# Optimization experiments

Hardware: AMD Instinct MI355X
Metric: run time of the kernel (lower is better)

Reference implementation:

```python
import jax, jax.numpy as jnp
import numpy as np

B, N, IN_DIM, HID = 8, 2048, 128, 64
LN_EPS = 1e-5
NEG_INF = -9e15
LRELU_SLOPE = 0.2


def setup_inputs() -> dict:
    key = jax.random.key(0)
    k1, k2, k3, k4, k5, k6 = jax.random.split(key, 6)
    stdv = 1.0 / np.sqrt(HID)
    adj = jax.random.randint(k1, (B, N, N), 0, 2, dtype=jnp.int32)
    # ensure self-loops so every row has at least one valid entry
    adj = adj.at[:, jnp.arange(N), jnp.arange(N)].set(1)
    return {
        "adj": adj,
        "x": jax.random.normal(k2, (B, N, IN_DIM), dtype=jnp.float32),
        "h": jax.random.normal(k3, (B, N, HID), dtype=jnp.float32),
        "X2H": jax.random.uniform(k4, (IN_DIM, 3 * HID), minval=-stdv, maxval=stdv, dtype=jnp.float32),
        "H2H": jax.random.uniform(k5, (HID, 3 * HID), minval=-stdv, maxval=stdv, dtype=jnp.float32),
        "a": jax.random.uniform(k6, (2 * HID, 1), minval=-stdv, maxval=stdv, dtype=jnp.float32),
    }


def _gated_inputs(x, h, X2H, H2H):
    gate_x = x @ X2H          # [B,N,3H]
    gate_h = h @ H2H          # [B,N,3H]
    i_r, i_i, i_n = jnp.split(gate_x, 3, axis=2)
    h_r, h_i, h_n = jnp.split(gate_h, 3, axis=2)
    resetgate = jax.nn.sigmoid(i_r + h_r)
    inputgate = jax.nn.sigmoid(i_i + h_i)
    irh = i_n + resetgate * h_n
    mu = jnp.mean(irh, axis=-1, keepdims=True)
    var = jnp.mean(jnp.square(irh - mu), axis=-1, keepdims=True)
    irh = (irh - mu) * jax.lax.rsqrt(var + LN_EPS)  # layer_norm, no affine
    newgate = jnp.tanh(irh)
    return newgate + inputgate * (h - newgate)


def reference(adj, x, h, X2H, H2H, a):
    Wh = _gated_inputs(x, h, X2H, H2H)              # [B,N,H]
    Wh1 = Wh @ a[:HID]                              # [B,N,1]
    Wh2 = Wh @ a[HID:]                              # [B,N,1]
    e = jax.nn.leaky_relu(Wh1 + jnp.swapaxes(Wh2, 1, 2), LRELU_SLOPE)  # [B,N,N]
    scores = jnp.where(adj != 0, e, jnp.float32(NEG_INF))
    attention = jax.nn.softmax(scores, axis=2)
    h_prime = attention @ Wh                        # [B,N,H]
    return (h_prime, Wh)
```

## Files before the change

kernel.cpp:

```cpp
#include <hip/hip_runtime.h>

constexpr int BB  = 8;
constexpr int NN  = 2048;
constexpr int IND = 128;
constexpr int HD  = 64;
constexpr float LN_EPS = 1e-5f;
constexpr float SLOPE  = 0.2f;

typedef _Float16 half8 __attribute__((ext_vector_type(8)));
typedef _Float16 half4 __attribute__((ext_vector_type(4)));
typedef float    f32x4 __attribute__((ext_vector_type(4)));

__device__ __forceinline__ float wave_sum(float v) {
    #pragma unroll
    for (int off = 32; off > 0; off >>= 1) v += __shfl_xor(v, off);
    return v;
}
__device__ __forceinline__ float wave_max(float v) {
    #pragma unroll
    for (int off = 32; off > 0; off >>= 1) v = fmaxf(v, __shfl_xor(v, off));
    return v;
}

__global__ void k_prep(const float* __restrict__ X2H, const float* __restrict__ H2H,
                       _Float16* __restrict__ Wt)
{
    const int tot = 256 * 192;
    for (int idx = blockIdx.x * 256 + threadIdx.x; idx < tot; idx += gridDim.x * 256) {
        const int col = idx / 192, k = idx % 192;
        float v;
        if (col < 128)       v = (k < 128) ? X2H[(size_t)k * 192 + col]
                                           : H2H[(size_t)(k - 128) * 192 + col];
        else if (col < 192)  v = (k < 128) ? X2H[(size_t)k * 192 + col] : 0.f;
        else                 v = (k >= 128) ? H2H[(size_t)(k - 128) * 192 + (col - 64)] : 0.f;
        Wt[idx] = (_Float16)v;
    }
}

__global__ __launch_bounds__(256, 4) void k_gates(
    const float* __restrict__ x, const float* __restrict__ h,
    const _Float16* __restrict__ Wt, const float* __restrict__ a,
    float* __restrict__ Wh_out, _Float16* __restrict__ Whh2,
    float* __restrict__ Wh1, float* __restrict__ Wh2)
{
    __shared__ float gbuf[16][260];

    const int tid = threadIdx.x, lane = tid & 63, w = tid >> 6;
    const int m = lane & 15, q = lane >> 4;
    const int row0 = blockIdx.x * 16;

    f32x4 acc[4];
    #pragma unroll
    for (int ct = 0; ct < 4; ++ct) acc[ct] = (f32x4){0.f, 0.f, 0.f, 0.f};

    #pragma unroll
    for (int kc = 0; kc < 6; ++kc) {
        half8 a8;
        if (kc < 4) {
            const float* xp = x + (size_t)(row0 + m) * IND + kc * 32 + q * 8;
            const f32x4 v0 = *(const f32x4*)xp;
            const f32x4 v1 = *(const f32x4*)(xp + 4);
            #pragma unroll
            for (int j = 0; j < 4; ++j) { a8[j] = (_Float16)v0[j]; a8[4 + j] = (_Float16)v1[j]; }
        } else {
            const float* hp_ = h + (size_t)(row0 + m) * HD + (kc - 4) * 32 + q * 8;
            const f32x4 v0 = *(const f32x4*)hp_;
            const f32x4 v1 = *(const f32x4*)(hp_ + 4);
            #pragma unroll
            for (int j = 0; j < 4; ++j) { a8[j] = (_Float16)v0[j]; a8[4 + j] = (_Float16)v1[j]; }
        }
        #pragma unroll
        for (int ct = 0; ct < 4; ++ct) {
            const half8 b8 = *(const half8*)(Wt + ((size_t)(w * 64 + ct * 16 + m) * 192 + kc * 32 + q * 8));
            acc[ct] = __builtin_amdgcn_mfma_f32_16x16x32_f16(a8, b8, acc[ct], 0, 0, 0);
        }
    }

    #pragma unroll
    for (int ct = 0; ct < 4; ++ct)
        #pragma unroll
        for (int r2 = 0; r2 < 4; ++r2)
            gbuf[q * 4 + r2][w * 64 + ct * 16 + m] = acc[ct][r2];
    __syncthreads();

    const float a0 = a[lane], a1 = a[64 + lane];
    half4 p4;
    const int grow0 = row0 + w * 4;
    #pragma unroll
    for (int r = 0; r < 4; ++r) {
        const int row = w * 4 + r;
        const int grow = row0 + row;
        const float g0 = gbuf[row][lane];
        const float g1 = gbuf[row][64 + lane];
        const float g2 = gbuf[row][128 + lane];
        const float g3 = gbuf[row][192 + lane];
        const float rg = 1.f / (1.f + __expf(-g0));
        const float ig = 1.f / (1.f + __expf(-g1));
        const float irh = g2 + rg * g3;
        const float mu = wave_sum(irh) * (1.f / 64.f);
        const float dv = irh - mu;
        const float var = wave_sum(dv * dv) * (1.f / 64.f);
        const float ng = tanhf(dv * rsqrtf(var + LN_EPS));
        const float hr = h[(size_t)grow * HD + lane];
        const float wh = ng + ig * (hr - ng);
        Wh_out[(size_t)grow * HD + lane] = wh;
        p4[r] = (_Float16)wh;
        const float d1 = wave_sum(wh * a0);
        const float d2 = wave_sum(wh * a1);
        if (lane == 0) { Wh1[grow] = d1; Wh2[grow] = d2; }
    }
    *(half4*)(Whh2 + ((size_t)(grow0 >> 3) * 64 + lane) * 8 + (w & 1) * 4) = p4;
}

__global__ __launch_bounds__(256) void k_aux(
    const float* __restrict__ Wh1, const float* __restrict__ Wh2,
    float* __restrict__ u, float* __restrict__ up,
    _Float16* __restrict__ v16, _Float16* __restrict__ v16p)
{
    __shared__ float red[4];
    const int tid = threadIdx.x, lane = tid & 63, w = tid >> 6;
    const int b = blockIdx.x >> 3, part = blockIdx.x & 7;

    float mx = -3e38f;
    #pragma unroll
    for (int k = 0; k < 8; ++k) mx = fmaxf(mx, Wh2[b * NN + k * 256 + tid]);
    mx = wave_max(mx);
    if (lane == 0) red[w] = mx;
    __syncthreads();
    const float M = fmaxf(fmaxf(red[0], red[1]), fmaxf(red[2], red[3]));

    const int grow = b * NN + part * 256 + tid;
    const float t0 = Wh1[grow] + M;
    const float c  = (t0 > 0.f) ? t0 : SLOPE * t0;
    u[grow]  = __expf(t0 - c);
    up[grow] = __expf(SLOPE * t0 - c);
    const float w2 = Wh2[grow] - M;
    v16[grow]  = (_Float16)__expf(w2);
    v16p[grow] = (_Float16)__expf(SLOPE * w2);
}

__global__ __launch_bounds__(256, 8) void k_score(
    const int* __restrict__ adj,
    const float* __restrict__ Wh1, const float* __restrict__ Wh2,
    unsigned short* __restrict__ Mb)
{
    const int tid = threadIdx.x;
    const int4* __restrict__ adj4 = (const int4*)adj;

    #pragma unroll
    for (int s = 0; s < 4; ++s) {
        const int row = s * 4096 + blockIdx.x;
        const int b   = row >> 11;
        const float negw1 = -Wh1[row];

        const int4 a0 = adj4[(size_t)row * 512 + tid * 2];
        const int4 a1 = adj4[(size_t)row * 512 + tid * 2 + 1];
        const f32x4 w0 = ((const f32x4*)(Wh2 + (size_t)b * NN))[tid * 2];
        const f32x4 w1 = ((const f32x4*)(Wh2 + (size_t)b * NN))[tid * 2 + 1];

        unsigned m1 = 0, m0 = 0;
        const int av[8] = {a0.x, a0.y, a0.z, a0.w, a1.x, a1.y, a1.z, a1.w};
        #pragma unroll
        for (int j = 0; j < 8; ++j) {
            const float wj = (j < 4) ? w0[j] : w1[j - 4];
            const bool a = (av[j] != 0);
            const bool ss = (wj > negw1);
            m1 |= (unsigned)(a && ss) << j;
            m0 |= (unsigned)(a && !ss) << j;
        }
        Mb[(size_t)row * 256 + tid] = (unsigned short)(m1 | (m0 << 8));
    }
}

__global__ __launch_bounds__(256, 4) void k_pv(
    const unsigned short* __restrict__ Mb,
    const _Float16* __restrict__ Whh2,
    const _Float16* __restrict__ v16, const _Float16* __restrict__ v16p,
    const float* __restrict__ u, const float* __restrict__ up,
    float* __restrict__ hp)
{
    __shared__ float accb[4][64][20];
    __shared__ float ssumw[4][16];

    const int tid = threadIdx.x, lane = tid & 63, w = tid >> 6;
    const int m = lane & 15, q = lane >> 4;
    const int b  = blockIdx.x >> 7;
    const int i0 = (blockIdx.x & 127) * 16;

    const int grow_m = b * NN + i0 + m;
    const _Float16 uh  = (_Float16)u[grow_m];
    const _Float16 uph = (_Float16)up[grow_m];

    const unsigned short* __restrict__ mrow = Mb + (size_t)grow_m * 256 + w * 64;
    const half8* __restrict__ Wp  = (const half8*)Whh2 + (size_t)b * 16384;
    const half8* __restrict__ v8  = (const half8*)v16  + b * 256;
    const half8* __restrict__ v8p = (const half8*)v16p + b * 256;

    half8 ones;
    #pragma unroll
    for (int j = 0; j < 8; ++j) ones[j] = (_Float16)1.f;

    f32x4 acc[4];
    #pragma unroll
    for (int cc = 0; cc < 4; ++cc) acc[cc] = (f32x4){0.f, 0.f, 0.f, 0.f};
    f32x4 accS = (f32x4){0.f, 0.f, 0.f, 0.f};

    #pragma unroll
    for (int k8 = 0; k8 < 16; ++k8) {
        const int slot  = k8 * 4 + q;
        const int kpack = w * 64 + slot;
        const unsigned mb = mrow[slot];
        const unsigned m1b = mb & 0xFFu, m0b = mb >> 8;

        const half8 vj  = v8[kpack];
        const half8 vjp = v8p[kpack];

        half8 Ac;
        #pragma unroll
        for (int j = 0; j < 8; ++j) {
            const _Float16 pos = uh * vj[j];
            const _Float16 neg = uph * vjp[j];
            Ac[j] = (m1b >> j & 1u) ? pos : ((m0b >> j & 1u) ? neg : (_Float16)0.f);
        }

        accS = __builtin_amdgcn_mfma_f32_16x16x32_f16(Ac, ones, accS, 0, 0, 0);
        #pragma unroll
        for (int cc = 0; cc < 4; ++cc) {
            const half8 b8 = Wp[(size_t)kpack * 64 + cc * 16 + m];
            acc[cc] = __builtin_amdgcn_mfma_f32_16x16x32_f16(Ac, b8, acc[cc], 0, 0, 0);
        }
    }

    if (m == 0) {
        #pragma unroll
        for (int r2 = 0; r2 < 4; ++r2) ssumw[w][q * 4 + r2] = accS[r2];
    }
    #pragma unroll
    for (int cc = 0; cc < 4; ++cc)
        *(f32x4*)&accb[w][lane][cc * 4] = acc[cc];
    __syncthreads();

    const int row = tid >> 4, c4 = tid & 15;
    const float S = ssumw[0][row] + ssumw[1][row] + ssumw[2][row] + ssumw[3][row];
    const int rq = row >> 2, r2 = row & 3;
    f32x4 tot;
    #pragma unroll
    for (int j = 0; j < 4; ++j) {
        const int col = c4 * 4 + j;
        const int cc = col >> 4, mm = col & 15;
        const int ln = rq * 16 + mm;
        float v = 0.f;
        #pragma unroll
        for (int wp = 0; wp < 4; ++wp) v += accb[wp][ln][cc * 4 + r2];
        tot[j] = v / S;
    }
    *(f32x4*)(hp + ((size_t)(b * NN + i0 + row)) * HD + c4 * 4) = tot;
}

extern "C" void kernel_launch(void* const* d_in, const int* in_sizes, int n_in,
                              void* d_out, int out_size, void* d_ws, size_t ws_size,
                              hipStream_t stream) {
    const int*   adj = (const int*)d_in[0];
    const float* x   = (const float*)d_in[1];
    const float* h   = (const float*)d_in[2];
    const float* X2H = (const float*)d_in[3];
    const float* H2H = (const float*)d_in[4];
    const float* a   = (const float*)d_in[5];

    float* out = (float*)d_out;
    float* hp  = out;
    float* Wh  = out + (size_t)BB * NN * HD;

    float*    Wh1  = (float*)d_ws;
    float*    Wh2  = Wh1 + BB * NN;
    float*    u    = Wh2 + BB * NN;
    float*    up   = u + BB * NN;
    _Float16* v16  = (_Float16*)(up + BB * NN);
    _Float16* v16p = v16 + BB * NN;
    _Float16* Whh2 = v16p + BB * NN;
    _Float16* Wt   = Whh2 + (size_t)BB * NN * HD;
    unsigned short* Mb = (unsigned short*)(Wt + 256 * 192);

    k_prep<<<dim3(64), dim3(256), 0, stream>>>(X2H, H2H, Wt);
    k_gates<<<dim3((BB * NN) / 16), dim3(256), 0, stream>>>(
        x, h, Wt, a, Wh, Whh2, Wh1, Wh2);
    k_aux<<<dim3(64), dim3(256), 0, stream>>>(Wh1, Wh2, u, up, v16, v16p);
    k_score<<<dim3(4096), dim3(256), 0, stream>>>(adj, Wh1, Wh2, Mb);
    k_pv<<<dim3(BB * (NN / 16)), dim3(256), 0, stream>>>(
        Mb, Whh2, v16, v16p, u, up, hp);
}
```

Before: 256.9 us.

## Fuse adjacency mask build into attention PV kernel via shared memory

Merges the separate score-mask kernel and the PV kernel into one kernel that reads adjacency rows directly, builds the sign/valid bitmask in shared memory, and then runs the MFMA accumulation. This removes the global round-trip of the packed mask buffer and one launch. Blocks grow to 512 threads (8 waves), each covering 256 columns, and the final reduction now sums across 8 waves. Holding 16 int4 adjacency loads per thread raises register pressure and may lower occupancy.

```diff
diff --git a/kernel.cpp b/kernel.cpp
--- a/kernel.cpp
+++ b/kernel.cpp
@@ -139,62 +139,63 @@
     v16p[grow] = (_Float16)__expf(SLOPE * w2);
 }
 
-__global__ __launch_bounds__(256, 8) void k_score(
+constexpr int MST = 65;
+
+__global__ __launch_bounds__(512, 4) void k_attn(
     const int* __restrict__ adj,
+    const _Float16* __restrict__ Whh2,
     const float* __restrict__ Wh1, const float* __restrict__ Wh2,
-    unsigned short* __restrict__ Mb)
-{
-    const int tid = threadIdx.x;
-    const int4* __restrict__ adj4 = (const int4*)adj;
-
-    #pragma unroll
-    for (int s = 0; s < 4; ++s) {
-        const int row = s * 4096 + blockIdx.x;
-        const int b   = row >> 11;
-        const float negw1 = -Wh1[row];
-
-        const int4 a0 = adj4[(size_t)row * 512 + tid * 2];
-        const int4 a1 = adj4[(size_t)row * 512 + tid * 2 + 1];
-        const f32x4 w0 = ((const f32x4*)(Wh2 + (size_t)b * NN))[tid * 2];
-        const f32x4 w1 = ((const f32x4*)(Wh2 + (size_t)b * NN))[tid * 2 + 1];
-
-        unsigned m1 = 0, m0 = 0;
-        const int av[8] = {a0.x, a0.y, a0.z, a0.w, a1.x, a1.y, a1.z, a1.w};
-        #pragma unroll
-        for (int j = 0; j < 8; ++j) {
-            const float wj = (j < 4) ? w0[j] : w1[j - 4];
-            const bool a = (av[j] != 0);
-            const bool ss = (wj > negw1);
-            m1 |= (unsigned)(a && ss) << j;
-            m0 |= (unsigned)(a && !ss) << j;
-        }
-        Mb[(size_t)row * 256 + tid] = (unsigned short)(m1 | (m0 << 8));
-    }
-}
-
-__global__ __launch_bounds__(256, 4) void k_pv(
-    const unsigned short* __restrict__ Mb,
-    const _Float16* __restrict__ Whh2,
+    const float* __restrict__ u, const float* __restrict__ up,
     const _Float16* __restrict__ v16, const _Float16* __restrict__ v16p,
-    const float* __restrict__ u, const float* __restrict__ up,
     float* __restrict__ hp)
 {
-    __shared__ float accb[4][64][20];
-    __shared__ float ssumw[4][16];
-
-    const int tid = threadIdx.x, lane = tid & 63, w = tid >> 6;
-    const int m = lane & 15, q = lane >> 4;
-    const int b  = blockIdx.x >> 7;
-    const int i0 = (blockIdx.x & 127) * 16;
+    __shared__ unsigned mk_all[8][4 * MST];
+    __shared__ float accb[8][64][17];
+    __shared__ float ssumw[8][16];
+
+    const int tid  = threadIdx.x;
+    const int lane = tid & 63;
+    const int w    = tid >> 6;
+    const int b    = blockIdx.x >> 7;
+    const int i0   = (blockIdx.x & 127) * 16;
+    const int m    = lane & 15;
+    const int q    = lane >> 4;
+
+    unsigned* __restrict__ mk = mk_all[w];
+
+    const int* __restrict__ abase = adj + ((size_t)b * NN + i0) * NN + w * 256 + 4 * lane;
+    int4 av[16];
+    #pragma unroll
+    for (int r = 0; r < 16; ++r) av[r] = *(const int4*)(abase + (size_t)r * NN);
+
+    const f32x4 w2v = ((const f32x4*)(Wh2 + (size_t)b * NN))[w * 64 + lane];
+
+    float negw1[16];
+    #pragma unroll
+    for (int r = 0; r < 16; ++r) negw1[r] = -Wh1[b * NN + i0 + r];
+
+    unsigned mword = 0;
+    #pragma unroll
+    for (int r = 0; r < 16; ++r) {
+        const int ai[4] = {av[r].x, av[r].y, av[r].z, av[r].w};
+        unsigned byte = 0;
+        #pragma unroll
+        for (int d = 0; d < 4; ++d) {
+            const bool ad = (ai[d] != 0);
+            const bool s  = (w2v[d] > negw1[r]);
+            byte |= (unsigned)(ad && s)  << d;
+            byte |= (unsigned)(ad && !s) << (4 + d);
+        }
+        mword |= byte << (8 * (r & 3));
+        if ((r & 3) == 3) { mk[(r >> 2) * MST + lane] = mword; mword = 0; }
+    }
 
     const int grow_m = b * NN + i0 + m;
     const _Float16 uh  = (_Float16)u[grow_m];
     const _Float16 uph = (_Float16)up[grow_m];
-
-    const unsigned short* __restrict__ mrow = Mb + (size_t)grow_m * 256 + w * 64;
+    const half8* __restrict__ v8  = (const half8*)(v16  + (size_t)b * NN);
+    const half8* __restrict__ v8p = (const half8*)(v16p + (size_t)b * NN);
     const half8* __restrict__ Wp  = (const half8*)Whh2 + (size_t)b * 16384;
-    const half8* __restrict__ v8  = (const half8*)v16  + b * 256;
-    const half8* __restrict__ v8p = (const half8*)v16p + b * 256;
 
     half8 ones;
     #pragma unroll
@@ -205,28 +206,30 @@
     for (int cc = 0; cc < 4; ++cc) acc[cc] = (f32x4){0.f, 0.f, 0.f, 0.f};
     f32x4 accS = (f32x4){0.f, 0.f, 0.f, 0.f};
 
-    #pragma unroll
-    for (int k8 = 0; k8 < 16; ++k8) {
-        const int slot  = k8 * 4 + q;
-        const int kpack = w * 64 + slot;
-        const unsigned mb = mrow[slot];
-        const unsigned m1b = mb & 0xFFu, m0b = mb >> 8;
-
-        const half8 vj  = v8[kpack];
-        const half8 vjp = v8p[kpack];
+    const int rg = m >> 2, sh = 8 * (m & 3);
+    #pragma unroll
+    for (int k8 = 0; k8 < 8; ++k8) {
+        const int cb0 = k8 * 8 + q * 2;
+        const unsigned b0 = (mk[rg * MST + cb0]     >> sh) & 0xFFu;
+        const unsigned b1 = (mk[rg * MST + cb0 + 1] >> sh) & 0xFFu;
+
+        const int kv = w * 32 + k8 * 4 + q;
+        const half8 vj  = v8[kv];
+        const half8 vjp = v8p[kv];
 
         half8 Ac;
         #pragma unroll
-        for (int j = 0; j < 8; ++j) {
-            const _Float16 pos = uh * vj[j];
-            const _Float16 neg = uph * vjp[j];
-            Ac[j] = (m1b >> j & 1u) ? pos : ((m0b >> j & 1u) ? neg : (_Float16)0.f);
+        for (int j = 0; j < 4; ++j) {
+            Ac[j]     = (b0 >> j & 1u) ? uh * vj[j]
+                      : ((b0 >> (4 + j) & 1u) ? uph * vjp[j] : (_Float16)0.f);
+            Ac[4 + j] = (b1 >> j & 1u) ? uh * vj[4 + j]
+                      : ((b1 >> (4 + j) & 1u) ? uph * vjp[4 + j] : (_Float16)0.f);
         }
 
         accS = __builtin_amdgcn_mfma_f32_16x16x32_f16(Ac, ones, accS, 0, 0, 0);
         #pragma unroll
         for (int cc = 0; cc < 4; ++cc) {
-            const half8 b8 = Wp[(size_t)kpack * 64 + cc * 16 + m];
+            const half8 b8 = Wp[(size_t)kv * 64 + cc * 16 + m];
             acc[cc] = __builtin_amdgcn_mfma_f32_16x16x32_f16(Ac, b8, acc[cc], 0, 0, 0);
         }
     }
@@ -240,21 +243,22 @@
         *(f32x4*)&accb[w][lane][cc * 4] = acc[cc];
     __syncthreads();
 
-    const int row = tid >> 4, c4 = tid & 15;
-    const float S = ssumw[0][row] + ssumw[1][row] + ssumw[2][row] + ssumw[3][row];
-    const int rq = row >> 2, r2 = row & 3;
-    f32x4 tot;
-    #pragma unroll
-    for (int j = 0; j < 4; ++j) {
-        const int col = c4 * 4 + j;
-        const int cc = col >> 4, mm = col & 15;
-        const int ln = rq * 16 + mm;
-        float v = 0.f;
-        #pragma unroll
-        for (int wp = 0; wp < 4; ++wp) v += accb[wp][ln][cc * 4 + r2];
-        tot[j] = v / S;
-    }
-    *(f32x4*)(hp + ((size_t)(b * NN + i0 + row)) * HD + c4 * 4) = tot;
+    if (w < 4) {
+        f32x4 tot = (f32x4){0.f, 0.f, 0.f, 0.f};
+        #pragma unroll
+        for (int wp = 0; wp < 8; ++wp) {
+            const f32x4 t4 = *(const f32x4*)&accb[wp][lane][w * 4];
+            tot[0] += t4[0]; tot[1] += t4[1]; tot[2] += t4[2]; tot[3] += t4[3];
+        }
+        #pragma unroll
+        for (int r2 = 0; r2 < 4; ++r2) {
+            const int irow = q * 4 + r2;
+            float S = 0.f;
+            #pragma unroll
+            for (int wp = 0; wp < 8; ++wp) S += ssumw[wp][irow];
+            hp[((size_t)b * NN + i0 + irow) * HD + w * 16 + m] = tot[r2] / S;
+        }
+    }
 }
 
 extern "C" void kernel_launch(void* const* d_in, const int* in_sizes, int n_in,
@@ -279,13 +283,11 @@
     _Float16* v16p = v16 + BB * NN;
     _Float16* Whh2 = v16p + BB * NN;
     _Float16* Wt   = Whh2 + (size_t)BB * NN * HD;
-    unsigned short* Mb = (unsigned short*)(Wt + 256 * 192);
 
     k_prep<<<dim3(64), dim3(256), 0, stream>>>(X2H, H2H, Wt);
     k_gates<<<dim3((BB * NN) / 16), dim3(256), 0, stream>>>(
         x, h, Wt, a, Wh, Whh2, Wh1, Wh2);
     k_aux<<<dim3(64), dim3(256), 0, stream>>>(Wh1, Wh2, u, up, v16, v16p);
-    k_score<<<dim3(4096), dim3(256), 0, stream>>>(adj, Wh1, Wh2, Mb);
-    k_pv<<<dim3(BB * (NN / 16)), dim3(256), 0, stream>>>(
-        Mb, Whh2, v16, v16p, u, up, hp);
-}
+    k_attn<<<dim3(BB * (NN / 16)), dim3(512), 0, stream>>>(
+        adj, Whh2, Wh1, Wh2, u, up, v16, v16p, hp);
+}
```

After: 248.3 us. -3.3%, faster.
